# Kernel tuning notes

Hardware: AMD Instinct MI355X
Metric: run time of the kernel (lower is better)

Reference implementation:

```python
import jax, jax.numpy as jnp
import numpy as np

NUM_HEADS = 6
WS = 3

def setup_inputs() -> dict:
    key = jax.random.key(0)
    k1, k2, k3 = jax.random.split(key, 3)
    dim = 192
    x = jax.random.normal(k1, (2, dim, 48, 48, 48), dtype=jnp.float32)
    Wqkv = jax.random.normal(k2, (3 * dim, dim), dtype=jnp.float32) * (dim ** -0.5)
    Wproj = jax.random.normal(k3, (dim, dim), dtype=jnp.float32) * (dim ** -0.5)
    bproj = jnp.zeros((dim,), dtype=jnp.float32)
    return {"x": x, "Wqkv": Wqkv, "Wproj": Wproj, "bproj": bproj, "H": 384, "W": 288}

def reference(x, Wqkv, Wproj, bproj, H, W):
    b, c, h, w, d = x.shape
    xt = x.reshape(b, -1, c)                      # (B, N, C) with C = c, N = h*w*d
    B, N, C = xt.shape
    nh, ws = NUM_HEADS, WS
    hd = C // nh
    scale = hd ** -0.5
    hg, wg = H // ws, W // ws
    tg = hg * wg
    # window partition: (B, hg, ws, wg, ws, C) -> (B, hg, wg, ws, ws, C)
    xw = xt.reshape(B, hg, ws, wg, ws, C).transpose(0, 1, 3, 2, 4, 5)
    # fused QKV projection (no bias)
    qkv = jnp.einsum('bgvijc,oc->bgvijo', xw, Wqkv)          # (B,hg,wg,ws,ws,3C)
    qkv = qkv.reshape(B, tg, ws * ws, 3, nh, hd).transpose(3, 0, 1, 4, 2, 5)
    q, k, v = qkv[0], qkv[1], qkv[2]                          # (B, tg, nh, 9, hd)
    attn = jnp.einsum('bgnqd,bgnkd->bgnqk', q, k) * scale     # (B, tg, nh, 9, 9)
    attn = jax.nn.softmax(attn, axis=-1)
    out = jnp.einsum('bgnqk,bgnkd->bgnqd', attn, v)           # (B, tg, nh, 9, hd)
    out = out.transpose(0, 1, 3, 2, 4).reshape(B, hg, wg, ws, ws, C)
    out = jnp.swapaxes(out, 2, 3).reshape(B, N, C)            # un-window
    out = out @ Wproj.T + bproj
    return out.reshape(b, c, h, w, d)
```

## Files before the change

### kernel.cpp

```cpp
#include <hip/hip_runtime.h>

typedef _Float16 f16;
typedef _Float16 f16x4 __attribute__((ext_vector_type(4)));
typedef _Float16 f16x8 __attribute__((ext_vector_type(8)));
typedef float f32x4 __attribute__((ext_vector_type(4)));

#define TPB  768
#define TPBF 576
#define NWIN 16
#define XS   200
#define WSS  200
#define QS   40
#define VS   264

#define WSQ_HALVES_PER_HEAD (96 * 200)
#define WSP_HALVES_PER_HEAD (192 * 40)
#define WS_NEEDED (230400 + 92160)

__device__ __forceinline__ void gload16(const void* g, void* l) {
    __builtin_amdgcn_global_load_lds(
        (const __attribute__((address_space(1))) unsigned int*)g,
        (__attribute__((address_space(3))) unsigned int*)l, 16, 0, 0);
}

__global__ __launch_bounds__(512) void conv_w(
    const float* __restrict__ Wqkv, const float* __restrict__ Wproj,
    f16* __restrict__ wsWq, f16* __restrict__ wsWp)
{
    int idx = blockIdx.x * 512 + threadIdx.x;
    if (idx < 110592) {
        int h = idx / (96 * 192), rem = idx % (96 * 192);
        int r = rem / 192, c = rem % 192;
        int grow = (r >> 5) * 192 + h * 32 + (r & 31);
        wsWq[(h * 96 + r) * 200 + c] = (f16)Wqkv[grow * 192 + c];
    } else {
        int j = idx - 110592;
        int h = j / (192 * 32), rem = j % (192 * 32);
        int r = rem / 32, c = rem % 32;
        wsWp[(h * 192 + r) * 40 + c] = (f16)Wproj[r * 192 + h * 32 + c];
    }
}

__global__ __launch_bounds__(TPB) void lsa_mfma14(
    const float* __restrict__ x, const f16* __restrict__ wsWq,
    const f16* __restrict__ wsWp, const float* __restrict__ bproj,
    float* __restrict__ out)
{
    __shared__ __attribute__((aligned(16))) f16 Xh[144 * XS];
    __shared__ __attribute__((aligned(16))) f16 Wh[96 * WSS];
    __shared__ __attribute__((aligned(16))) f16 Qh[144 * QS];
    __shared__ __attribute__((aligned(16))) f16 Kh[144 * QS];
    __shared__ __attribute__((aligned(16))) f16 Vt2[32 * VS];
    __shared__ __attribute__((aligned(16))) f16 AOh[144 * QS];
    __shared__ __attribute__((aligned(16))) f16 Wp[192 * QS];

    const int tid  = threadIdx.x;
    const int lane = tid & 63;
    const int w    = tid >> 6;
    const int ci   = w % 3;
    const int tg   = w / 3;
    const int l15  = lane & 15;
    const int lg   = lane >> 4;

    const int  bb    = blockIdx.x / 768;
    const int  gbase = (blockIdx.x % 768) * NWIN;
    const long rb0   = (long)bb * 110592 + (long)(gbase / 96) * 864 + (long)(gbase % 96) * 3;

    for (int l = tid; l < 2400; l += TPB)
        gload16(wsWq + l * 8, (char*)Wh + l * 16);
    for (int i = 0; i < 9; ++i) {
        int idx = i * TPB + tid;
        int t = idx / 48, c4 = idx % 48;
        int wi = t / 9, q = t - 9 * wi;
        long grow = rb0 + wi * 3 + (q / 3) * 288 + (q % 3);
        float4 xv = ((const float4*)x)[grow * 48 + c4];
        union { f16 h[4]; ushort4 u; } tmp;
        tmp.h[0] = (f16)xv.x; tmp.h[1] = (f16)xv.y; tmp.h[2] = (f16)xv.z; tmp.h[3] = (f16)xv.w;
        *(ushort4*)&Xh[t * XS + c4 * 4] = tmp.u;
    }
    {
        int4 z = {0, 0, 0, 0};
        for (int i2 = tid; i2 < (32 * VS * 2) / 16; i2 += TPB) ((int4*)Vt2)[i2] = z;
    }

    f32x4 pacc[9];
    #pragma unroll
    for (int a = 0; a < 9; ++a) pacc[a] = (f32x4){0.f, 0.f, 0.f, 0.f};

    __syncthreads();

    for (int h = 0; h < 6; ++h) {
        f32x4 qacc[2][3];
        #pragma unroll
        for (int c = 0; c < 2; ++c)
            #pragma unroll
            for (int t = 0; t < 3; ++t)
                qacc[c][t] = (f32x4){0.f, 0.f, 0.f, 0.f};
        #pragma unroll
        for (int kk = 0; kk < 6; ++kk) {
            f16x8 af[2];
            af[0] = *(const f16x8*)&Wh[(16 * ci        + l15) * WSS + kk * 32 + lg * 8];
            af[1] = *(const f16x8*)&Wh[(16 * (ci + 3)  + l15) * WSS + kk * 32 + lg * 8];
            #pragma unroll
            for (int t = 0; t < 3; ++t) {
                int tt = tg + 4 * t;
                if (tt < 9) {
                    f16x8 bf = *(const f16x8*)&Xh[(16 * tt + l15) * XS + kk * 32 + lg * 8];
                    qacc[0][t] = __builtin_amdgcn_mfma_f32_16x16x32_f16(af[0], bf, qacc[0][t], 0, 0, 0);
                    qacc[1][t] = __builtin_amdgcn_mfma_f32_16x16x32_f16(af[1], bf, qacc[1][t], 0, 0, 0);
                }
            }
        }
        #pragma unroll
        for (int c = 0; c < 2; ++c) {
            const int ct = ci + 3 * c;
            #pragma unroll
            for (int t = 0; t < 3; ++t) {
                int tt = tg + 4 * t;
                if (tt < 9) {
                    const int token = 16 * tt + l15;
                    f16x4 ph;
                    ph[0] = (f16)qacc[c][t][0]; ph[1] = (f16)qacc[c][t][1];
                    ph[2] = (f16)qacc[c][t][2]; ph[3] = (f16)qacc[c][t][3];
                    if (ct < 2) {
                        *(f16x4*)&Qh[token * QS + ct * 16 + 4 * lg] = ph;
                    } else if (ct < 4) {
                        *(f16x4*)&Kh[token * QS + (ct - 2) * 16 + 4 * lg] = ph;
                    } else {
                        const int d0 = (ct - 4) * 16 + 4 * lg;
                        int wi = token / 9, qq = token - 9 * wi;
                        #pragma unroll
                        for (int r = 0; r < 4; ++r)
                            Vt2[(d0 + r) * VS + 16 * wi + qq] = ph[r];
                    }
                }
            }
        }
        __syncthreads();

        if (h < 5) {
            for (int l = tid; l < 2400; l += TPB)
                gload16(wsWq + (h + 1) * WSQ_HALVES_PER_HEAD + l * 8, (char*)Wh + l * 16);
        }
        for (int l = tid; l < 960; l += TPB)
            gload16(wsWp + h * WSP_HALVES_PER_HEAD + l * 8, (char*)Wp + l * 16);

        for (int wi = w; wi < NWIN; wi += 12) {
            int krow = 9 * wi + l15;
            krow = krow > 143 ? 143 : krow;
            f16x8 ak = *(const f16x8*)&Kh[krow * QS + lg * 8];
            f16x8 aq = *(const f16x8*)&Qh[krow * QS + lg * 8];
            f32x4 s = (f32x4){0.f, 0.f, 0.f, 0.f};
            s = __builtin_amdgcn_mfma_f32_16x16x32_f16(ak, aq, s, 0, 0, 0);
            float lgt[4];
            float mx = -1e30f;
            #pragma unroll
            for (int r = 0; r < 4; ++r) {
                int kx = 4 * lg + r;
                lgt[r] = (kx < 9) ? s[r] * 0.17677669529663687f : -1e30f;
                mx = fmaxf(mx, lgt[r]);
            }
            mx = fmaxf(mx, __shfl_xor(mx, 16));
            mx = fmaxf(mx, __shfl_xor(mx, 32));
            float e[4], sum = 0.f;
            #pragma unroll
            for (int r = 0; r < 4; ++r) {
                int kx = 4 * lg + r;
                e[r] = (kx < 9) ? __expf(lgt[r] - mx) : 0.f;
                sum += e[r];
            }
            sum += __shfl_xor(sum, 16);
            sum += __shfl_xor(sum, 32);
            float inv = 1.0f / sum;
            f16x4 p;
            p[0] = (f16)(e[0] * inv); p[1] = (f16)(e[1] * inv);
            p[2] = (f16)(e[2] * inv); p[3] = (f16)(e[3] * inv);
            #pragma unroll
            for (int dt = 0; dt < 2; ++dt) {
                f16x4 av = *(const f16x4*)&Vt2[(dt * 16 + l15) * VS + 16 * wi + 4 * lg];
                f32x4 o = (f32x4){0.f, 0.f, 0.f, 0.f};
                o = __builtin_amdgcn_mfma_f32_16x16x16f16(av, p, o, 0, 0, 0);
                if (l15 < 9) {
                    f16x4 oh;
                    oh[0] = (f16)o[0]; oh[1] = (f16)o[1]; oh[2] = (f16)o[2]; oh[3] = (f16)o[3];
                    *(f16x4*)&AOh[(9 * wi + l15) * QS + dt * 16 + 4 * lg] = oh;
                }
            }
        }
        __syncthreads();

        {
            f16x8 bw = *(const f16x8*)&Wp[(16 * w + l15) * QS + lg * 8];
            #pragma unroll
            for (int a = 0; a < 9; ++a) {
                f16x8 aof = *(const f16x8*)&AOh[(16 * a + l15) * QS + lg * 8];
                pacc[a] = __builtin_amdgcn_mfma_f32_16x16x32_f16(aof, bw, pacc[a], 0, 0, 0);
            }
        }
    }

    const float bv = bproj[16 * w + l15];
    #pragma unroll
    for (int a = 0; a < 9; ++a) {
        #pragma unroll
        for (int r = 0; r < 4; ++r) {
            int t = 16 * a + lg * 4 + r;
            int wi = t / 9, q = t - 9 * wi;
            long grow = rb0 + wi * 3 + (q / 3) * 288 + (q % 3);
            out[grow * 192 + 16 * w + l15] = pacc[a][r] + bv;
        }
    }
}

__global__ __launch_bounds__(TPBF) void lsa_mfma7(
    const float* __restrict__ x, const float* __restrict__ Wqkv,
    const float* __restrict__ Wproj, const float* __restrict__ bproj,
    float* __restrict__ out)
{
    __shared__ f16 Xh[144 * XS];
    __shared__ f16 Wh[96 * WSS];
    __shared__ f16 Qh[144 * QS];
    __shared__ f16 Kh[144 * QS];
    __shared__ f16 Vt2[32 * VS];
    __shared__ f16 AOh[144 * QS];
    __shared__ f16 Wp[192 * QS];

    const int tid  = threadIdx.x;
    const int lane = tid & 63;
    const int w    = tid >> 6;
    const int ci   = w / 3;
    const int ti   = w % 3;
    const int l15  = lane & 15;
    const int lg   = lane >> 4;

    const int  bb    = blockIdx.x / 768;
    const int  gbase = (blockIdx.x % 768) * NWIN;
    const long rb0   = (long)bb * 110592 + (long)(gbase / 96) * 864 + (long)(gbase % 96) * 3;

    const float4* Wq4 = (const float4*)Wqkv;
    const float4* Wp4 = (const float4*)Wproj;

    for (int idx = tid; idx < 144 * 48; idx += TPBF) {
        int t = idx / 48, c4 = idx % 48;
        int wi = t / 9, q = t - 9 * wi;
        long grow = rb0 + wi * 3 + (q / 3) * 288 + (q % 3);
        float4 xv = ((const float4*)x)[grow * 48 + c4];
        union { f16 h[4]; ushort4 u; } tmp;
        tmp.h[0] = (f16)xv.x; tmp.h[1] = (f16)xv.y; tmp.h[2] = (f16)xv.z; tmp.h[3] = (f16)xv.w;
        *(ushort4*)&Xh[t * XS + c4 * 4] = tmp.u;
    }
    {
        int4 z = {0, 0, 0, 0};
        for (int i2 = tid; i2 < (32 * VS * 2) / 16; i2 += TPBF) ((int4*)Vt2)[i2] = z;
    }
    #pragma unroll
    for (int i = 0; i < 8; ++i) {
        int l = i * TPBF + tid;
        int r = l / 48, c4 = l % 48;
        float4 wv = Wq4[((r >> 5) * 192 + (r & 31)) * 48 + c4];
        union { f16 h4[4]; ushort4 u; } t;
        t.h4[0] = (f16)wv.x; t.h4[1] = (f16)wv.y; t.h4[2] = (f16)wv.z; t.h4[3] = (f16)wv.w;
        *(ushort4*)&Wh[r * WSS + c4 * 4] = t.u;
    }

    f32x4 pacc[3][4];
    #pragma unroll
    for (int a = 0; a < 3; ++a)
        #pragma unroll
        for (int bq = 0; bq < 4; ++bq)
            pacc[a][bq] = (f32x4){0.f, 0.f, 0.f, 0.f};

    __syncthreads();

    for (int h = 0; h < 6; ++h) {
        f32x4 qacc[2][3];
        #pragma unroll
        for (int c = 0; c < 2; ++c)
            #pragma unroll
            for (int t = 0; t < 3; ++t)
                qacc[c][t] = (f32x4){0.f, 0.f, 0.f, 0.f};
        #pragma unroll
        for (int kk = 0; kk < 6; ++kk) {
            f16x8 af[2], bf[3];
            #pragma unroll
            for (int c = 0; c < 2; ++c)
                af[c] = *(const f16x8*)&Wh[(16 * (ci + 3 * c) + l15) * WSS + kk * 32 + lg * 8];
            #pragma unroll
            for (int t = 0; t < 3; ++t)
                bf[t] = *(const f16x8*)&Xh[(16 * (ti + 3 * t) + l15) * XS + kk * 32 + lg * 8];
            #pragma unroll
            for (int c = 0; c < 2; ++c)
                #pragma unroll
                for (int t = 0; t < 3; ++t)
                    qacc[c][t] = __builtin_amdgcn_mfma_f32_16x16x32_f16(af[c], bf[t], qacc[c][t], 0, 0, 0);
        }
        #pragma unroll
        for (int c = 0; c < 2; ++c) {
            const int ct = ci + 3 * c;
            #pragma unroll
            for (int t = 0; t < 3; ++t) {
                const int token = 16 * (ti + 3 * t) + l15;
                f16x4 ph;
                ph[0] = (f16)qacc[c][t][0]; ph[1] = (f16)qacc[c][t][1];
                ph[2] = (f16)qacc[c][t][2]; ph[3] = (f16)qacc[c][t][3];
                if (ct < 2) {
                    *(f16x4*)&Qh[token * QS + ct * 16 + 4 * lg] = ph;
                } else if (ct < 4) {
                    *(f16x4*)&Kh[token * QS + (ct - 2) * 16 + 4 * lg] = ph;
                } else {
                    const int d0 = (ct - 4) * 16 + 4 * lg;
                    int wi = token / 9, qq = token - 9 * wi;
                    #pragma unroll
                    for (int r = 0; r < 4; ++r)
                        Vt2[(d0 + r) * VS + 16 * wi + qq] = ph[r];
                }
            }
        }
        __syncthreads();

        float4 wpv[3];
        if (tid < 512) {
            #pragma unroll
            for (int i = 0; i < 3; ++i) {
                int l = i * 512 + tid;
                int r = l / 8, c4 = l % 8;
                wpv[i] = Wp4[r * 48 + h * 8 + c4];
            }
        }
        if (h < 5) {
            #pragma unroll
            for (int i = 0; i < 8; ++i) {
                int l = i * TPBF + tid;
                int r = l / 48, c4 = l % 48;
                float4 wv = Wq4[((r >> 5) * 192 + (h + 1) * 32 + (r & 31)) * 48 + c4];
                union { f16 h4[4]; ushort4 u; } t;
                t.h4[0] = (f16)wv.x; t.h4[1] = (f16)wv.y; t.h4[2] = (f16)wv.z; t.h4[3] = (f16)wv.w;
                *(ushort4*)&Wh[r * WSS + c4 * 4] = t.u;
            }
        }
        for (int wi = w; wi < NWIN; wi += 9) {
            int krow = 9 * wi + l15;
            krow = krow > 143 ? 143 : krow;
            f16x8 ak = *(const f16x8*)&Kh[krow * QS + lg * 8];
            f16x8 aq = *(const f16x8*)&Qh[krow * QS + lg * 8];
            f32x4 s = (f32x4){0.f, 0.f, 0.f, 0.f};
            s = __builtin_amdgcn_mfma_f32_16x16x32_f16(ak, aq, s, 0, 0, 0);
            float lgt[4];
            float mx = -1e30f;
            #pragma unroll
            for (int r = 0; r < 4; ++r) {
                int kx = 4 * lg + r;
                lgt[r] = (kx < 9) ? s[r] * 0.17677669529663687f : -1e30f;
                mx = fmaxf(mx, lgt[r]);
            }
            mx = fmaxf(mx, __shfl_xor(mx, 16));
            mx = fmaxf(mx, __shfl_xor(mx, 32));
            float e[4], sum = 0.f;
            #pragma unroll
            for (int r = 0; r < 4; ++r) {
                int kx = 4 * lg + r;
                e[r] = (kx < 9) ? __expf(lgt[r] - mx) : 0.f;
                sum += e[r];
            }
            sum += __shfl_xor(sum, 16);
            sum += __shfl_xor(sum, 32);
            float inv = 1.0f / sum;
            f16x4 p;
            p[0] = (f16)(e[0] * inv); p[1] = (f16)(e[1] * inv);
            p[2] = (f16)(e[2] * inv); p[3] = (f16)(e[3] * inv);
            #pragma unroll
            for (int dt = 0; dt < 2; ++dt) {
                f16x4 av = *(const f16x4*)&Vt2[(dt * 16 + l15) * VS + 16 * wi + 4 * lg];
                f32x4 o = (f32x4){0.f, 0.f, 0.f, 0.f};
                o = __builtin_amdgcn_mfma_f32_16x16x16f16(av, p, o, 0, 0, 0);
                if (l15 < 9) {
                    f16x4 oh;
                    oh[0] = (f16)o[0]; oh[1] = (f16)o[1]; oh[2] = (f16)o[2]; oh[3] = (f16)o[3];
                    *(f16x4*)&AOh[(9 * wi + l15) * QS + dt * 16 + 4 * lg] = oh;
                }
            }
        }
        if (tid < 512) {
            #pragma unroll
            for (int i = 0; i < 3; ++i) {
                int l = i * 512 + tid;
                int r = l / 8, c4 = l % 8;
                union { f16 h4[4]; ushort4 u; } t;
                t.h4[0] = (f16)wpv[i].x; t.h4[1] = (f16)wpv[i].y;
                t.h4[2] = (f16)wpv[i].z; t.h4[3] = (f16)wpv[i].w;
                *(ushort4*)&Wp[r * QS + c4 * 4] = t.u;
            }
        }
        __syncthreads();

        {
            f16x8 aof[3];
            #pragma unroll
            for (int a = 0; a < 3; ++a)
                aof[a] = *(const f16x8*)&AOh[(16 * (3 * ci + a) + l15) * QS + lg * 8];
            #pragma unroll
            for (int bq = 0; bq < 4; ++bq) {
                f16x8 bw = *(const f16x8*)&Wp[(16 * (4 * ti + bq) + l15) * QS + lg * 8];
                #pragma unroll
                for (int a = 0; a < 3; ++a)
                    pacc[a][bq] = __builtin_amdgcn_mfma_f32_16x16x32_f16(aof[a], bw, pacc[a][bq], 0, 0, 0);
            }
        }
    }

    float bv[4];
    #pragma unroll
    for (int bq = 0; bq < 4; ++bq)
        bv[bq] = bproj[16 * (4 * ti + bq) + l15];
    #pragma unroll
    for (int a = 0; a < 3; ++a) {
        #pragma unroll
        for (int r = 0; r < 4; ++r) {
            int t = 16 * (3 * ci + a) + lg * 4 + r;
            int wi = t / 9, q = t - 9 * wi;
            long grow = rb0 + wi * 3 + (q / 3) * 288 + (q % 3);
            float* dst = out + grow * 192;
            #pragma unroll
            for (int bq = 0; bq < 4; ++bq)
                dst[16 * (4 * ti + bq) + l15] = pacc[a][bq][r] + bv[bq];
        }
    }
}

extern "C" void kernel_launch(void* const* d_in, const int* in_sizes, int n_in,
                              void* d_out, int out_size, void* d_ws, size_t ws_size,
                              hipStream_t stream) {
    const float* x     = (const float*)d_in[0];
    const float* Wqkv  = (const float*)d_in[1];
    const float* Wproj = (const float*)d_in[2];
    const float* bproj = (const float*)d_in[3];
    float* out = (float*)d_out;
    if (ws_size >= (size_t)WS_NEEDED && d_ws != nullptr) {
        f16* wsWq = (f16*)d_ws;
        f16* wsWp = (f16*)((char*)d_ws + 230400);
        conv_w<<<288, 512, 0, stream>>>(Wqkv, Wproj, wsWq, wsWp);
        lsa_mfma14<<<1536, TPB, 0, stream>>>(x, wsWq, wsWp, bproj, out);
    } else {
        lsa_mfma7<<<1536, TPBF, 0, stream>>>(x, Wqkv, Wproj, bproj, out);
    }
}
```

Baseline: 198.3 us.

## Load QKV weight fragments directly from global in MFMA-fragment order

The conversion kernel now writes the fp16 QKV weights pre-swizzled into per-lane MFMA A-fragment order, so each wave reads its 16-byte fragment straight from global/L2 with a coalesced load. This removes the Wh shared-memory buffer and the per-head async copies into it, which frees LDS and cuts LDS traffic. The trade-off is that each of the 12 waves now fetches its weight fragments from global memory inside the inner MFMA loop, adding L2 latency to the QKV projection.

```diff
diff --git a/kernel.cpp b/kernel.cpp
--- a/kernel.cpp
+++ b/kernel.cpp
@@ -13,9 +13,9 @@
 #define QS   40
 #define VS   264
 
-#define WSQ_HALVES_PER_HEAD (96 * 200)
+#define WSQF_HALVES 110592
 #define WSP_HALVES_PER_HEAD (192 * 40)
-#define WS_NEEDED (230400 + 92160)
+#define WS_NEEDED (221184 + 92160)
 
 __device__ __forceinline__ void gload16(const void* g, void* l) {
     __builtin_amdgcn_global_load_lds(
@@ -25,29 +25,36 @@
 
 __global__ __launch_bounds__(512) void conv_w(
     const float* __restrict__ Wqkv, const float* __restrict__ Wproj,
-    f16* __restrict__ wsWq, f16* __restrict__ wsWp)
+    f16* __restrict__ wsWqf, f16* __restrict__ wsWp)
 {
     int idx = blockIdx.x * 512 + threadIdx.x;
-    if (idx < 110592) {
-        int h = idx / (96 * 192), rem = idx % (96 * 192);
-        int r = rem / 192, c = rem % 192;
+    if (idx < WSQF_HALVES) {
+        int h    = idx / 18432;
+        int rem  = idx % 18432;
+        int ct   = rem / 3072;
+        int rem2 = rem % 3072;
+        int kk   = rem2 / 512;
+        int rem3 = rem2 % 512;
+        int lane = rem3 / 8;
+        int e    = rem3 % 8;
+        int r    = 16 * ct + (lane & 15);
         int grow = (r >> 5) * 192 + h * 32 + (r & 31);
-        wsWq[(h * 96 + r) * 200 + c] = (f16)Wqkv[grow * 192 + c];
+        int col  = kk * 32 + (lane >> 4) * 8 + e;
+        wsWqf[idx] = (f16)Wqkv[grow * 192 + col];
     } else {
-        int j = idx - 110592;
+        int j = idx - WSQF_HALVES;
         int h = j / (192 * 32), rem = j % (192 * 32);
         int r = rem / 32, c = rem % 32;
         wsWp[(h * 192 + r) * 40 + c] = (f16)Wproj[r * 192 + h * 32 + c];
     }
 }
 
-__global__ __launch_bounds__(TPB) void lsa_mfma14(
-    const float* __restrict__ x, const f16* __restrict__ wsWq,
+__global__ __launch_bounds__(TPB) void lsa_mfma16(
+    const float* __restrict__ x, const f16* __restrict__ wsWqf,
     const f16* __restrict__ wsWp, const float* __restrict__ bproj,
     float* __restrict__ out)
 {
     __shared__ __attribute__((aligned(16))) f16 Xh[144 * XS];
-    __shared__ __attribute__((aligned(16))) f16 Wh[96 * WSS];
     __shared__ __attribute__((aligned(16))) f16 Qh[144 * QS];
     __shared__ __attribute__((aligned(16))) f16 Kh[144 * QS];
     __shared__ __attribute__((aligned(16))) f16 Vt2[32 * VS];
@@ -66,8 +73,8 @@
     const int  gbase = (blockIdx.x % 768) * NWIN;
     const long rb0   = (long)bb * 110592 + (long)(gbase / 96) * 864 + (long)(gbase % 96) * 3;
 
-    for (int l = tid; l < 2400; l += TPB)
-        gload16(wsWq + l * 8, (char*)Wh + l * 16);
+    const f16x8* wqf = (const f16x8*)wsWqf;
+
     for (int i = 0; i < 9; ++i) {
         int idx = i * TPB + tid;
         int t = idx / 48, c4 = idx % 48;
@@ -99,8 +106,8 @@
         #pragma unroll
         for (int kk = 0; kk < 6; ++kk) {
             f16x8 af[2];
-            af[0] = *(const f16x8*)&Wh[(16 * ci        + l15) * WSS + kk * 32 + lg * 8];
-            af[1] = *(const f16x8*)&Wh[(16 * (ci + 3)  + l15) * WSS + kk * 32 + lg * 8];
+            af[0] = wqf[((h * 6 + ci    ) * 6 + kk) * 64 + lane];
+            af[1] = wqf[((h * 6 + ci + 3) * 6 + kk) * 64 + lane];
             #pragma unroll
             for (int t = 0; t < 3; ++t) {
                 int tt = tg + 4 * t;
@@ -138,10 +145,6 @@
         }
         __syncthreads();
 
-        if (h < 5) {
-            for (int l = tid; l < 2400; l += TPB)
-                gload16(wsWq + (h + 1) * WSQ_HALVES_PER_HEAD + l * 8, (char*)Wh + l * 16);
-        }
         for (int l = tid; l < 960; l += TPB)
             gload16(wsWp + h * WSP_HALVES_PER_HEAD + l * 8, (char*)Wp + l * 16);
 
@@ -436,10 +439,10 @@
     const float* bproj = (const float*)d_in[3];
     float* out = (float*)d_out;
     if (ws_size >= (size_t)WS_NEEDED && d_ws != nullptr) {
-        f16* wsWq = (f16*)d_ws;
-        f16* wsWp = (f16*)((char*)d_ws + 230400);
-        conv_w<<<288, 512, 0, stream>>>(Wqkv, Wproj, wsWq, wsWp);
-        lsa_mfma14<<<1536, TPB, 0, stream>>>(x, wsWq, wsWp, bproj, out);
+        f16* wsWqf = (f16*)d_ws;
+        f16* wsWp  = (f16*)((char*)d_ws + 221184);
+        conv_w<<<288, 512, 0, stream>>>(Wqkv, Wproj, wsWqf, wsWp);
+        lsa_mfma16<<<1536, TPB, 0, stream>>>(x, wsWqf, wsWp, bproj, out);
     } else {
         lsa_mfma7<<<1536, TPBF, 0, stream>>>(x, Wqkv, Wproj, bproj, out);
     }
```

New measurement: 229.5 us. +15.7%, slower.
